# Performance work log

Measured on AMD Instinct MI355X. Metric: run time of the kernel, lower is better.

## Reference

```python
import jax, jax.numpy as jnp
import numpy as np

HIDDEN = 20
VOCAB = 29
NUM_LAYERS = 1
SEQ_LEN = 64
BATCH = 16384


def setup_inputs() -> dict:
    key = jax.random.key(0)
    k1, k2, k3, k4, k5 = jax.random.split(key, 5)
    return {
        "x": jax.random.normal(k1, (SEQ_LEN, BATCH, VOCAB), dtype=jnp.float32),
        "img_emb": jax.random.normal(k2, (BATCH, HIDDEN), dtype=jnp.float32),
        "W_ih": jax.random.normal(k3, (NUM_LAYERS, HIDDEN, VOCAB), dtype=jnp.float32),
        "b_ih": jnp.zeros((NUM_LAYERS, HIDDEN), dtype=jnp.float32),
        "W_hh": jax.random.normal(k4, (NUM_LAYERS, HIDDEN, HIDDEN), dtype=jnp.float32),
        "b_hh": jnp.zeros((NUM_LAYERS, HIDDEN), dtype=jnp.float32),
        "W_ho": jax.random.normal(k5, (VOCAB, HIDDEN), dtype=jnp.float32),
        "b_ho": jnp.zeros((VOCAB,), dtype=jnp.float32),
    }


def reference(x, img_emb, W_ih, b_ih, W_hh, b_hh, W_ho, b_ho):
    # num_layers == 1: take layer 0 weights
    Wi, bi = W_ih[0], b_ih[0]   # [H,V], [H]
    Wh, bh = W_hh[0], b_hh[0]   # [H,H], [H]
    seq_len, batch = x.shape[0], x.shape[1]
    # img_emb is only added at t == 0
    first = (jnp.arange(seq_len) == 0).astype(x.dtype)  # [T]

    def step(h, inp):
        xt, f = inp  # xt: [B,V], f: scalar
        h_new = jnp.tanh(xt @ Wi.T + bi + h @ Wh.T + bh + f * img_emb)
        return h_new, h_new

    h0 = jnp.zeros((batch, Wi.shape[0]), dtype=x.dtype)
    _, hs = jax.lax.scan(step, h0, (x, first))  # hs: [T,B,H]
    logits = hs @ W_ho.T + b_ho  # [T,B,V]
    return jax.nn.log_softmax(logits, axis=-1)
```

## Files before the change

### kernel.cpp

```cpp
#include <hip/hip_runtime.h>

#define Tn 64
#define Bn 16384
#define Vn 29
#define Hn 20

typedef float f4 __attribute__((ext_vector_type(4)));

static __device__ __forceinline__ f4 ld4u(const float* p) {
  f4 v; __builtin_memcpy(&v, p, 16); return v;
}
static __device__ __forceinline__ void st4u(float* p, f4 v) {
  __builtin_memcpy(p, &v, 16);
}

#define LOG2E 1.4426950408889634f
#define LN2   0.6931471805599453f

static __device__ __forceinline__ float frcp(float x) {
#if __has_builtin(__builtin_amdgcn_rcpf)
  return __builtin_amdgcn_rcpf(x);
#else
  return 1.0f / x;
#endif
}
static __device__ __forceinline__ float fexp2(float x) {
#if __has_builtin(__builtin_amdgcn_exp2f)
  return __builtin_amdgcn_exp2f(x);
#else
  return exp2f(x);
#endif
}
static __device__ __forceinline__ float flog2(float x) {
#if __has_builtin(__builtin_amdgcn_logf)
  return __builtin_amdgcn_logf(x);
#else
  return log2f(x);
#endif
}
static __device__ __forceinline__ float ftanh(float x) {
  float e = fexp2(x * (2.0f * LOG2E));
  return 1.0f - 2.0f * frcp(1.0f + e);
}

#define SWZ(v, imm) __int_as_float(__builtin_amdgcn_ds_swizzle(__float_as_int(v), (imm)))
#define PAT(ow) (((ow) << 5) | 0x18)

__global__ __launch_bounds__(256, 3) void k_pre(
    const float* __restrict__ x, const float* __restrict__ img,
    const float* __restrict__ Wi, const float* __restrict__ bih,
    const float* __restrict__ bhh, float* __restrict__ xi)
{
  __shared__ f4 sW[Hn * 8];
  __shared__ float sB[Hn];
  float* sWf = (float*)sW;
  const int tid = threadIdx.x;
  for (int i = tid; i < Hn * 32; i += 256) {
    int r = i >> 5, c = i & 31;
    sWf[i] = (c < Vn) ? Wi[r * Vn + c] : 0.0f;
  }
  if (tid < Hn) sB[tid] = bih[tid] + bhh[tid];
  __syncthreads();

  const int g  = blockIdx.x * 256 + tid;
  const int t  = g >> 13;
  const int b0 = (g & 8191) << 1;

  const float* xr = x + ((size_t)t * Bn + b0) * Vn;
  f4 xa[8], xb[8];
#pragma unroll
  for (int q = 0; q < 7; ++q) {
    xa[q] = ld4u(xr + 4 * q);
    xb[q] = ld4u(xr + Vn + 4 * q);
  }
  xa[7] = f4{xr[28], 0.0f, 0.0f, 0.0f};
  xb[7] = f4{xr[Vn + 28], 0.0f, 0.0f, 0.0f};

  const bool first = (t == 0);
  const float* ia = img + (size_t)b0 * Hn;
  float* orow = xi + ((size_t)t * Bn + b0) * Hn;

  float oa4[4], ob4[4];
#pragma unroll
  for (int h = 0; h < Hn; ++h) {
    float aa = sB[h], ab = sB[h];
#pragma unroll
    for (int q = 0; q < 8; ++q) {
      f4 w = sW[h * 8 + q];
      aa += w.x * xa[q].x + w.y * xa[q].y + w.z * xa[q].z + w.w * xa[q].w;
      ab += w.x * xb[q].x + w.y * xb[q].y + w.z * xb[q].z + w.w * xb[q].w;
    }
    if (first) { aa += ia[h]; ab += ia[Hn + h]; }
    oa4[h & 3] = aa; ob4[h & 3] = ab;
    if ((h & 3) == 3) {
      *(f4*)(orow + (h - 3))      = f4{oa4[0], oa4[1], oa4[2], oa4[3]};
      *(f4*)(orow + Hn + (h - 3)) = f4{ob4[0], ob4[1], ob4[2], ob4[3]};
    }
  }
}

__global__ __launch_bounds__(256, 2) void k_rnn(
    const float* __restrict__ xi, const float* __restrict__ Wh,
    const float* __restrict__ Who, const float* __restrict__ bho,
    float* __restrict__ out)
{
  const int gt = blockIdx.x * 256 + threadIdx.x;
  const int b = gt >> 3;
  const int j = gt & 7;

  float wh[3][Hn];
#pragma unroll
  for (int s = 0; s < 3; ++s) {
    int r = 3 * j + s; r = r > 19 ? 19 : r;
    const f4* wr = (const f4*)(Wh + r * Hn);
#pragma unroll
    for (int q = 0; q < 5; ++q) {
      f4 v = wr[q];
      wh[s][4*q] = v.x; wh[s][4*q+1] = v.y; wh[s][4*q+2] = v.z; wh[s][4*q+3] = v.w;
    }
  }
  float wo[4][Hn], bo[4];
#pragma unroll
  for (int rr = 0; rr < 4; ++rr) {
    int v = 4 * j + rr; int vc = v > 28 ? 28 : v;
    const f4* wr = (const f4*)(Who + vc * Hn);
#pragma unroll
    for (int q = 0; q < 5; ++q) {
      f4 w = wr[q];
      wo[rr][4*q] = w.x; wo[rr][4*q+1] = w.y; wo[rr][4*q+2] = w.z; wo[rr][4*q+3] = w.w;
    }
    bo[rr] = (v < Vn) ? bho[v] : -1e30f;
  }

  int c0 = 3 * j;     c0 = c0 > 19 ? 19 : c0;
  int c1 = 3 * j + 1; c1 = c1 > 19 ? 19 : c1;
  int c2 = 3 * j + 2; c2 = c2 > 19 ? 19 : c2;

  const float* xp = xi + (size_t)b * Hn;
  float nx0 = xp[c0], nx1 = xp[c1], nx2 = xp[c2];

  float hbc[Hn];
#pragma unroll
  for (int k = 0; k < Hn; ++k) hbc[k] = 0.0f;

  float* op = out + (size_t)b * Vn + 4 * j;
  const size_t xstep = (size_t)Bn * Hn;
  const size_t ostep = (size_t)Bn * Vn;

#pragma unroll 1
  for (int t = 0; t < Tn; ++t) {
    float a0 = nx0, a1 = nx1, a2 = nx2;
    xp += xstep;
    nx0 = xp[c0]; nx1 = xp[c1]; nx2 = xp[c2];

#pragma unroll
    for (int k = 0; k < Hn; ++k) {
      float hk = hbc[k];
      a0 += hk * wh[0][k]; a1 += hk * wh[1][k]; a2 += hk * wh[2][k];
    }
    float h0 = ftanh(a0), h1 = ftanh(a1), h2 = ftanh(a2);

    hbc[0]  = SWZ(h0, PAT(0)); hbc[1]  = SWZ(h1, PAT(0)); hbc[2]  = SWZ(h2, PAT(0));
    hbc[3]  = SWZ(h0, PAT(1)); hbc[4]  = SWZ(h1, PAT(1)); hbc[5]  = SWZ(h2, PAT(1));
    hbc[6]  = SWZ(h0, PAT(2)); hbc[7]  = SWZ(h1, PAT(2)); hbc[8]  = SWZ(h2, PAT(2));
    hbc[9]  = SWZ(h0, PAT(3)); hbc[10] = SWZ(h1, PAT(3)); hbc[11] = SWZ(h2, PAT(3));
    hbc[12] = SWZ(h0, PAT(4)); hbc[13] = SWZ(h1, PAT(4)); hbc[14] = SWZ(h2, PAT(4));
    hbc[15] = SWZ(h0, PAT(5)); hbc[16] = SWZ(h1, PAT(5)); hbc[17] = SWZ(h2, PAT(5));
    hbc[18] = SWZ(h0, PAT(6)); hbc[19] = SWZ(h1, PAT(6));

    float l0 = bo[0], l1 = bo[1], l2 = bo[2], l3 = bo[3];
#pragma unroll
    for (int k = 0; k < Hn; ++k) {
      float hk = hbc[k];
      l0 += hk * wo[0][k]; l1 += hk * wo[1][k];
      l2 += hk * wo[2][k]; l3 += hk * wo[3][k];
    }

    float m = fmaxf(fmaxf(l0, l1), fmaxf(l2, l3));
    m = fmaxf(m, SWZ(m, 0x041F));
    m = fmaxf(m, SWZ(m, 0x081F));
    m = fmaxf(m, SWZ(m, 0x101F));
    float e0 = fexp2((l0 - m) * LOG2E), e1 = fexp2((l1 - m) * LOG2E);
    float e2 = fexp2((l2 - m) * LOG2E), e3 = fexp2((l3 - m) * LOG2E);
    float s = e0 + e1 + e2 + e3;
    s += SWZ(s, 0x041F);
    s += SWZ(s, 0x081F);
    s += SWZ(s, 0x101F);
    float ls = m + flog2(s) * LN2;

    f4 o = f4{l0 - ls, l1 - ls, l2 - ls, l3 - ls};
    if (j < 7) st4u(op, o);
    else       op[0] = l0 - ls;
    op += ostep;
  }
}

extern "C" void kernel_launch(void* const* d_in, const int* in_sizes, int n_in,
                              void* d_out, int out_size, void* d_ws, size_t ws_size,
                              hipStream_t stream)
{
  const float* x   = (const float*)d_in[0];
  const float* img = (const float*)d_in[1];
  const float* Wi  = (const float*)d_in[2];
  const float* bi  = (const float*)d_in[3];
  const float* Wh  = (const float*)d_in[4];
  const float* bh  = (const float*)d_in[5];
  const float* Who = (const float*)d_in[6];
  const float* bho = (const float*)d_in[7];
  float* out = (float*)d_out;
  float* xi  = (float*)d_ws;

  k_pre<<<(Tn * Bn / 2) / 256, 256, 0, stream>>>(x, img, Wi, bi, bh, xi);
  k_rnn<<<(8 * Bn) / 256, 256, 0, stream>>>(xi, Wh, Who, bho, out);
}
```

Measured before the change: 316.1 us.

## Split RNN into pre, recurrence, and output kernels with DPP broadcast

The fused recurrence-plus-output kernel becomes three kernels. The input projection now uses one thread per (t,b) and reads weights directly from global/scalar memory. The recurrence uses 4 lanes per batch element, each owning 5 hidden units, broadcasts h through DPP quad permutes, prefetches three steps ahead, and writes h back in place into the workspace. A separate fully parallel kernel computes the output projection and log-softmax. This shortens the serial recurrence loop, at the cost of an extra HBM round trip for the hidden states and one more launch.

```diff
diff --git a/kernel.cpp b/kernel.cpp
--- a/kernel.cpp
+++ b/kernel.cpp
@@ -43,156 +43,150 @@
   return 1.0f - 2.0f * frcp(1.0f + e);
 }
 
-#define SWZ(v, imm) __int_as_float(__builtin_amdgcn_ds_swizzle(__float_as_int(v), (imm)))
-#define PAT(ow) (((ow) << 5) | 0x18)
-
-__global__ __launch_bounds__(256, 3) void k_pre(
+#define DPPF(v, ctrl) __int_as_float(__builtin_amdgcn_update_dpp( \
+    0, __float_as_int(v), (ctrl), 0xF, 0xF, true))
+#define DPPB(v, j) DPPF(v, ((j) == 0 ? 0x00 : ((j) == 1 ? 0x55 : ((j) == 2 ? 0xAA : 0xFF))))
+
+__global__ __launch_bounds__(256) void k_pre(
     const float* __restrict__ x, const float* __restrict__ img,
-    const float* __restrict__ Wi, const float* __restrict__ bih,
-    const float* __restrict__ bhh, float* __restrict__ xi)
-{
-  __shared__ f4 sW[Hn * 8];
-  __shared__ float sB[Hn];
-  float* sWf = (float*)sW;
-  const int tid = threadIdx.x;
-  for (int i = tid; i < Hn * 32; i += 256) {
-    int r = i >> 5, c = i & 31;
-    sWf[i] = (c < Vn) ? Wi[r * Vn + c] : 0.0f;
-  }
-  if (tid < Hn) sB[tid] = bih[tid] + bhh[tid];
-  __syncthreads();
-
-  const int g  = blockIdx.x * 256 + tid;
-  const int t  = g >> 13;
-  const int b0 = (g & 8191) << 1;
-
-  const float* xr = x + ((size_t)t * Bn + b0) * Vn;
-  f4 xa[8], xb[8];
+    const float* __restrict__ Wi, const float* __restrict__ bi,
+    const float* __restrict__ bh, float* __restrict__ xi)
+{
+  const int e = blockIdx.x * 256 + threadIdx.x;
+  const int t = e >> 14;
+  const int b = e & (Bn - 1);
+
+  const float* xr = x + (size_t)e * Vn;
+  float xv[Vn];
 #pragma unroll
   for (int q = 0; q < 7; ++q) {
-    xa[q] = ld4u(xr + 4 * q);
-    xb[q] = ld4u(xr + Vn + 4 * q);
-  }
-  xa[7] = f4{xr[28], 0.0f, 0.0f, 0.0f};
-  xb[7] = f4{xr[Vn + 28], 0.0f, 0.0f, 0.0f};
+    f4 v = ld4u(xr + 4 * q);
+    xv[4*q] = v.x; xv[4*q+1] = v.y; xv[4*q+2] = v.z; xv[4*q+3] = v.w;
+  }
+  xv[28] = xr[28];
 
   const bool first = (t == 0);
-  const float* ia = img + (size_t)b0 * Hn;
-  float* orow = xi + ((size_t)t * Bn + b0) * Hn;
-
-  float oa4[4], ob4[4];
-#pragma unroll
-  for (int h = 0; h < Hn; ++h) {
-    float aa = sB[h], ab = sB[h];
-#pragma unroll
-    for (int q = 0; q < 8; ++q) {
-      f4 w = sW[h * 8 + q];
-      aa += w.x * xa[q].x + w.y * xa[q].y + w.z * xa[q].z + w.w * xa[q].w;
-      ab += w.x * xb[q].x + w.y * xb[q].y + w.z * xb[q].z + w.w * xb[q].w;
+  const float* ia = img + (size_t)b * Hn;
+  float* orow = xi + (size_t)e * Hn;
+
+#pragma unroll
+  for (int hb = 0; hb < 5; ++hb) {
+    float acc[4];
+#pragma unroll
+    for (int r = 0; r < 4; ++r) {
+      const int h = hb * 4 + r;
+      float a = bi[h] + bh[h];
+#pragma unroll
+      for (int k = 0; k < Vn; ++k)
+        a += Wi[h * Vn + k] * xv[k];
+      acc[r] = a;
     }
-    if (first) { aa += ia[h]; ab += ia[Hn + h]; }
-    oa4[h & 3] = aa; ob4[h & 3] = ab;
-    if ((h & 3) == 3) {
-      *(f4*)(orow + (h - 3))      = f4{oa4[0], oa4[1], oa4[2], oa4[3]};
-      *(f4*)(orow + Hn + (h - 3)) = f4{ob4[0], ob4[1], ob4[2], ob4[3]};
+    if (first) {
+      f4 iv = *(const f4*)(ia + hb * 4);
+      acc[0] += iv.x; acc[1] += iv.y; acc[2] += iv.z; acc[3] += iv.w;
     }
-  }
-}
-
-__global__ __launch_bounds__(256, 2) void k_rnn(
-    const float* __restrict__ xi, const float* __restrict__ Wh,
-    const float* __restrict__ Who, const float* __restrict__ bho,
-    float* __restrict__ out)
+    st4u(orow + hb * 4, f4{acc[0], acc[1], acc[2], acc[3]});
+  }
+}
+
+#define HSEL4(k) ((k) % 5 == 0 ? hr0 : ((k) % 5 == 1 ? hr1 : \
+                  ((k) % 5 == 2 ? hr2 : ((k) % 5 == 3 ? hr3 : hr4))))
+#define WH4_STEP(k) { float hk_ = DPPB(HSEL4(k), (k) / 5); \
+  a0 += hk_ * wh0[(k)]; a1 += hk_ * wh1[(k)]; a2 += hk_ * wh2[(k)]; \
+  a3 += hk_ * wh3[(k)]; a4 += hk_ * wh4[(k)]; }
+#define WH4_ALL \
+  WH4_STEP(0)  WH4_STEP(1)  WH4_STEP(2)  WH4_STEP(3)  WH4_STEP(4)  \
+  WH4_STEP(5)  WH4_STEP(6)  WH4_STEP(7)  WH4_STEP(8)  WH4_STEP(9)  \
+  WH4_STEP(10) WH4_STEP(11) WH4_STEP(12) WH4_STEP(13) WH4_STEP(14) \
+  WH4_STEP(15) WH4_STEP(16) WH4_STEP(17) WH4_STEP(18) WH4_STEP(19)
+
+__global__ __launch_bounds__(256) void k_rec(
+    float* __restrict__ ws, const float* __restrict__ Wh)
 {
   const int gt = blockIdx.x * 256 + threadIdx.x;
-  const int b = gt >> 3;
-  const int j = gt & 7;
-
-  float wh[3][Hn];
-#pragma unroll
-  for (int s = 0; s < 3; ++s) {
-    int r = 3 * j + s; r = r > 19 ? 19 : r;
-    const f4* wr = (const f4*)(Wh + r * Hn);
-#pragma unroll
-    for (int q = 0; q < 5; ++q) {
-      f4 v = wr[q];
-      wh[s][4*q] = v.x; wh[s][4*q+1] = v.y; wh[s][4*q+2] = v.z; wh[s][4*q+3] = v.w;
-    }
-  }
-  float wo[4][Hn], bo[4];
-#pragma unroll
-  for (int rr = 0; rr < 4; ++rr) {
-    int v = 4 * j + rr; int vc = v > 28 ? 28 : v;
-    const f4* wr = (const f4*)(Who + vc * Hn);
-#pragma unroll
-    for (int q = 0; q < 5; ++q) {
-      f4 w = wr[q];
-      wo[rr][4*q] = w.x; wo[rr][4*q+1] = w.y; wo[rr][4*q+2] = w.z; wo[rr][4*q+3] = w.w;
-    }
-    bo[rr] = (v < Vn) ? bho[v] : -1e30f;
-  }
-
-  int c0 = 3 * j;     c0 = c0 > 19 ? 19 : c0;
-  int c1 = 3 * j + 1; c1 = c1 > 19 ? 19 : c1;
-  int c2 = 3 * j + 2; c2 = c2 > 19 ? 19 : c2;
-
-  const float* xp = xi + (size_t)b * Hn;
-  float nx0 = xp[c0], nx1 = xp[c1], nx2 = xp[c2];
-
-  float hbc[Hn];
-#pragma unroll
-  for (int k = 0; k < Hn; ++k) hbc[k] = 0.0f;
-
-  float* op = out + (size_t)b * Vn + 4 * j;
-  const size_t xstep = (size_t)Bn * Hn;
-  const size_t ostep = (size_t)Bn * Vn;
+  const int b = gt >> 2;
+  const int j = gt & 3;
+
+  float wh0[Hn], wh1[Hn], wh2[Hn], wh3[Hn], wh4[Hn];
+#pragma unroll
+  for (int q = 0; q < 5; ++q) {
+    f4 v0 = *(const f4*)(Wh + (5*j+0) * Hn + 4*q);
+    f4 v1 = *(const f4*)(Wh + (5*j+1) * Hn + 4*q);
+    f4 v2 = *(const f4*)(Wh + (5*j+2) * Hn + 4*q);
+    f4 v3 = *(const f4*)(Wh + (5*j+3) * Hn + 4*q);
+    f4 v4 = *(const f4*)(Wh + (5*j+4) * Hn + 4*q);
+    wh0[4*q]=v0.x; wh0[4*q+1]=v0.y; wh0[4*q+2]=v0.z; wh0[4*q+3]=v0.w;
+    wh1[4*q]=v1.x; wh1[4*q+1]=v1.y; wh1[4*q+2]=v1.z; wh1[4*q+3]=v1.w;
+    wh2[4*q]=v2.x; wh2[4*q+1]=v2.y; wh2[4*q+2]=v2.z; wh2[4*q+3]=v2.w;
+    wh3[4*q]=v3.x; wh3[4*q+1]=v3.y; wh3[4*q+2]=v3.z; wh3[4*q+3]=v3.w;
+    wh4[4*q]=v4.x; wh4[4*q+1]=v4.y; wh4[4*q+2]=v4.z; wh4[4*q+3]=v4.w;
+  }
+
+  float* p = ws + (size_t)b * Hn + 5 * j;
+  const size_t step = (size_t)Bn * Hn;
+
+  f4 c4 = ld4u(p);              float c1 = p[4];
+  f4 n4 = ld4u(p + step);       float n1 = p[4 + step];
+  f4 m4 = ld4u(p + 2 * step);   float m1 = p[4 + 2 * step];
+  const float* pf = p + 3 * step;
+
+  float hr0 = 0.f, hr1 = 0.f, hr2 = 0.f, hr3 = 0.f, hr4 = 0.f;
 
 #pragma unroll 1
   for (int t = 0; t < Tn; ++t) {
-    float a0 = nx0, a1 = nx1, a2 = nx2;
-    xp += xstep;
-    nx0 = xp[c0]; nx1 = xp[c1]; nx2 = xp[c2];
-
-#pragma unroll
-    for (int k = 0; k < Hn; ++k) {
-      float hk = hbc[k];
-      a0 += hk * wh[0][k]; a1 += hk * wh[1][k]; a2 += hk * wh[2][k];
-    }
-    float h0 = ftanh(a0), h1 = ftanh(a1), h2 = ftanh(a2);
-
-    hbc[0]  = SWZ(h0, PAT(0)); hbc[1]  = SWZ(h1, PAT(0)); hbc[2]  = SWZ(h2, PAT(0));
-    hbc[3]  = SWZ(h0, PAT(1)); hbc[4]  = SWZ(h1, PAT(1)); hbc[5]  = SWZ(h2, PAT(1));
-    hbc[6]  = SWZ(h0, PAT(2)); hbc[7]  = SWZ(h1, PAT(2)); hbc[8]  = SWZ(h2, PAT(2));
-    hbc[9]  = SWZ(h0, PAT(3)); hbc[10] = SWZ(h1, PAT(3)); hbc[11] = SWZ(h2, PAT(3));
-    hbc[12] = SWZ(h0, PAT(4)); hbc[13] = SWZ(h1, PAT(4)); hbc[14] = SWZ(h2, PAT(4));
-    hbc[15] = SWZ(h0, PAT(5)); hbc[16] = SWZ(h1, PAT(5)); hbc[17] = SWZ(h2, PAT(5));
-    hbc[18] = SWZ(h0, PAT(6)); hbc[19] = SWZ(h1, PAT(6));
-
-    float l0 = bo[0], l1 = bo[1], l2 = bo[2], l3 = bo[3];
-#pragma unroll
-    for (int k = 0; k < Hn; ++k) {
-      float hk = hbc[k];
-      l0 += hk * wo[0][k]; l1 += hk * wo[1][k];
-      l2 += hk * wo[2][k]; l3 += hk * wo[3][k];
-    }
-
-    float m = fmaxf(fmaxf(l0, l1), fmaxf(l2, l3));
-    m = fmaxf(m, SWZ(m, 0x041F));
-    m = fmaxf(m, SWZ(m, 0x081F));
-    m = fmaxf(m, SWZ(m, 0x101F));
-    float e0 = fexp2((l0 - m) * LOG2E), e1 = fexp2((l1 - m) * LOG2E);
-    float e2 = fexp2((l2 - m) * LOG2E), e3 = fexp2((l3 - m) * LOG2E);
-    float s = e0 + e1 + e2 + e3;
-    s += SWZ(s, 0x041F);
-    s += SWZ(s, 0x081F);
-    s += SWZ(s, 0x101F);
-    float ls = m + flog2(s) * LN2;
-
-    f4 o = f4{l0 - ls, l1 - ls, l2 - ls, l3 - ls};
-    if (j < 7) st4u(op, o);
-    else       op[0] = l0 - ls;
-    op += ostep;
-  }
+    f4 q4 = c4; float q1 = 0.f;
+    if (t < Tn - 3) { q4 = ld4u(pf); q1 = pf[4]; pf += step; }
+
+    float a0 = c4.x, a1 = c4.y, a2 = c4.z, a3 = c4.w, a4 = c1;
+    WH4_ALL
+    hr0 = ftanh(a0); hr1 = ftanh(a1); hr2 = ftanh(a2);
+    hr3 = ftanh(a3); hr4 = ftanh(a4);
+
+    st4u(p, f4{hr0, hr1, hr2, hr3});
+    p[4] = hr4;
+    p += step;
+
+    c4 = n4; c1 = n1; n4 = m4; n1 = m1; m4 = q4; m1 = q1;
+  }
+}
+
+__global__ __launch_bounds__(256) void k_out(
+    const float* __restrict__ hs, const float* __restrict__ Who,
+    const float* __restrict__ bho, float* __restrict__ out)
+{
+  const size_t e = (size_t)blockIdx.x * 256 + threadIdx.x;
+
+  const float* hp = hs + e * Hn;
+  float hv[Hn];
+#pragma unroll
+  for (int q = 0; q < 5; ++q) {
+    f4 v = *(const f4*)(hp + 4 * q);
+    hv[4*q] = v.x; hv[4*q+1] = v.y; hv[4*q+2] = v.z; hv[4*q+3] = v.w;
+  }
+
+  float lg[Vn];
+#pragma unroll
+  for (int v = 0; v < Vn; ++v) {
+    float a = bho[v];
+#pragma unroll
+    for (int k = 0; k < Hn; ++k)
+      a += Who[v * Hn + k] * hv[k];
+    lg[v] = a;
+  }
+
+  float m = lg[0];
+#pragma unroll
+  for (int v = 1; v < Vn; ++v) m = fmaxf(m, lg[v]);
+  float s = 0.f;
+#pragma unroll
+  for (int v = 0; v < Vn; ++v) s += fexp2((lg[v] - m) * LOG2E);
+  const float ls = m + flog2(s) * LN2;
+
+  float* op = out + e * Vn;
+#pragma unroll
+  for (int q = 0; q < 7; ++q)
+    st4u(op + 4 * q, f4{lg[4*q] - ls, lg[4*q+1] - ls, lg[4*q+2] - ls, lg[4*q+3] - ls});
+  op[28] = lg[28] - ls;
 }
 
 extern "C" void kernel_launch(void* const* d_in, const int* in_sizes, int n_in,
@@ -208,8 +202,9 @@
   const float* Who = (const float*)d_in[6];
   const float* bho = (const float*)d_in[7];
   float* out = (float*)d_out;
-  float* xi  = (float*)d_ws;
-
-  k_pre<<<(Tn * Bn / 2) / 256, 256, 0, stream>>>(x, img, Wi, bi, bh, xi);
-  k_rnn<<<(8 * Bn) / 256, 256, 0, stream>>>(xi, Wh, Who, bho, out);
-}
+  float* ws  = (float*)d_ws;
+
+  k_pre<<<(Tn * Bn) / 256, 256, 0, stream>>>(x, img, Wi, bi, bh, ws);
+  k_rec<<<(4 * Bn) / 256, 256, 0, stream>>>(ws, Wh);
+  k_out<<<(Tn * Bn) / 256, 256, 0, stream>>>(ws, Who, bho, out);
+}
```

New measurement: 335.2 us. 1.06x slower.
